# Kernel optimization log

Measured on AMD Instinct MI355X. Metric: run time of the kernel, lower is better.

The kernel has to match this reference:

```python
import jax, jax.numpy as jnp
import numpy as np

B, L, D, H, DH, S_POKES = 1, 4096, 1024, 16, 64, 3072


def setup_inputs() -> dict:
    key = jax.random.key(0)
    k0, k1, k2, k3 = jax.random.split(key, 4)
    x = jax.random.normal(k0, (B, L, D), jnp.float32)
    pos = jax.random.uniform(k1, (B, L, 2), jnp.float32)  # positions in [0,1]^2
    qkv_w = jax.random.normal(k2, (3 * D, D), jnp.float32) * 0.02
    out_w = jax.random.normal(k3, (D, D), jnp.float32) * 0.02
    scale = jnp.ones((H,), jnp.float32) * 10.0  # per-head cosine-sim scale (init 10)
    # AxialRoPE2D freq table: logspace(pi, 10*pi), view(2, d_head//4, n_heads).mT
    n = H * DH // 4
    f = np.exp(np.linspace(np.log(np.pi), np.log(10.0 * np.pi), n + 1)[:-1])
    freqs = jnp.asarray(np.stack([f, f]).reshape(2, DH // 4, H).transpose(0, 2, 1), jnp.float32)
    return {"x": x, "pos": pos, "qkv_w": qkv_w, "out_w": out_w,
            "scale": scale, "freqs": freqs, "n_pokes": S_POKES}


def _cos_scale(q, k, scale, eps=1e-8):
    # scale_for_cosine_sim: qk logits = scale * cosine_similarity
    sq = jnp.sum(q * q, axis=-1, keepdims=True)
    sk = jnp.sum(k * k, axis=-1, keepdims=True)
    ss = jnp.sqrt(jnp.abs(scale) + eps)
    return q * (ss * jax.lax.rsqrt(sq + eps)), k * (ss * jax.lax.rsqrt(sk + eps))


def _axial_theta(pos, freqs):
    # pos [B,L,2] in [0,1]; theta [B,H,L,DH//2]
    th_w = (pos[..., None, 0:1] * 2.0 - 1.0) * freqs[0]  # [B,L,H,DH//4]
    th_h = (pos[..., None, 1:2] * 2.0 - 1.0) * freqs[1]
    return jnp.concatenate([th_h, th_w], axis=-1).transpose(0, 2, 1, 3)


def _rope(x, theta):
    d = theta.shape[-1]  # DH//2 -> rotates the full head dim, x3 part empty
    x1, x2 = x[..., :d], x[..., d:2 * d]
    cos, sin = jnp.cos(theta), jnp.sin(theta)
    return jnp.concatenate([x1 * cos - x2 * sin, x2 * cos + x1 * sin], axis=-1)


def reference(x, pos, qkv_w, out_w, scale, freqs, n_pokes):
    b, l, dm = x.shape
    qkv = x @ qkv_w.T                          # [B,L,3D]
    q, k, v = jnp.split(qkv, 3, axis=-1)
    split_heads = lambda t: t.reshape(b, l, H, DH).transpose(0, 2, 1, 3)  # [B,H,L,DH]
    q, k, v = split_heads(q), split_heads(k), split_heads(v)
    q, k = _cos_scale(q, k, scale.reshape(1, H, 1, 1))
    theta = _axial_theta(pos, freqs)
    q, k = _rope(q, theta), _rope(k, theta)
    s = n_pokes
    qp, kp, vp = q[:, :, :s], k[:, :, :s], v[:, :, :s]
    qq, kq, vq = q[:, :, s:], k[:, :, s:], v[:, :, s:]
    # pokes: causal self-attention (scale=1.0, cosine-sim logits)
    sc_pp = jnp.einsum('bhqd,bhkd->bhqk', qp, kp)
    causal = jnp.tril(jnp.ones((s, s), bool))
    p_pp = jax.nn.softmax(jnp.where(causal, sc_pp, -jnp.inf), axis=-1)
    out_p = jnp.einsum('bhqk,bhkd->bhqd', p_pp, vp)
    # queries: attend to all pokes + themselves (diagonal), never each other
    sc_qp = jnp.einsum('bhqd,bhkd->bhqk', qq, kp)          # [B,H,Q,S]
    sc_self = jnp.sum(qq * kq, axis=-1, keepdims=True)     # [B,H,Q,1]
    p_q = jax.nn.softmax(jnp.concatenate([sc_qp, sc_self], axis=-1), axis=-1)
    out_q = jnp.einsum('bhqk,bhkd->bhqd', p_q[..., :s], vp) + p_q[..., s:] * vq
    out = jnp.concatenate([out_p, out_q], axis=2).transpose(0, 2, 1, 3).reshape(b, l, dm)
    return out @ out_w.T
```

## Files before the change

### kernel.cpp

```cpp
#include <hip/hip_runtime.h>
#include <math.h>

#define SEQL   4096
#define DMODEL 1024
#define NH     16
#define DHEAD  64
#define SPOKES 3072
#define NQUERY (SEQL - SPOKES)
#define QKVN   (3 * DMODEL)
#define LOG2E  1.4426950408889634f

typedef short bf16x8 __attribute__((ext_vector_type(8)));
typedef short bf16x4 __attribute__((ext_vector_type(4)));
typedef float f32x4  __attribute__((ext_vector_type(4)));

__device__ __forceinline__ short f2bf(float f) {
    unsigned u = __builtin_bit_cast(unsigned, f);
    u += 0x7fffu + ((u >> 16) & 1u);
    return (short)(u >> 16);
}
__device__ __forceinline__ float bf2f(short s) {
    unsigned u = ((unsigned)(unsigned short)s) << 16;
    return __builtin_bit_cast(float, u);
}
__device__ __forceinline__ unsigned cvt_pk_bf16(float lo, float hi) {
    unsigned u;
    asm("v_cvt_pk_bf16_f32 %0, %1, %2" : "=v"(u) : "v"(lo), "v"(hi));
    return u;
}
__device__ __forceinline__ float fast_exp2(float x) {
#if __has_builtin(__builtin_amdgcn_exp2f)
    return __builtin_amdgcn_exp2f(x);
#else
    float r; asm("v_exp_f32 %0, %1" : "=v"(r) : "v"(x)); return r;
#endif
}
__device__ __forceinline__ int swz(int row) { return ((row & 7) ^ (row >> 3)) << 4; }

__device__ __forceinline__ void gload_lds16(const void* g, void* l) {
    __builtin_amdgcn_global_load_lds(
        (const __attribute__((address_space(1))) unsigned int*)g,
        (__attribute__((address_space(3))) unsigned int*)l,
        16, 0, 0);
}

#define CVT_N0 (SEQL * DMODEL / 8)
#define CVT_N1 (QKVN * DMODEL / 8)
#define CVT_N2 (DMODEL * DMODEL / 8)
__global__ __launch_bounds__(256) void cvt_all(
    const float* __restrict__ x, const float* __restrict__ wq, const float* __restrict__ wo,
    short* __restrict__ xb, short* __restrict__ wqb, short* __restrict__ wob)
{
    int i = blockIdx.x * 256 + threadIdx.x;
    const float* src; short* dst;
    if (i < CVT_N0)               { src = x;  dst = xb; }
    else if (i < CVT_N0 + CVT_N1) { src = wq; dst = wqb; i -= CVT_N0; }
    else                          { src = wo; dst = wob; i -= CVT_N0 + CVT_N1; }
    float4 a = ((const float4*)src)[i * 2];
    float4 b = ((const float4*)src)[i * 2 + 1];
    bf16x8 v;
    v[0] = f2bf(a.x); v[1] = f2bf(a.y); v[2] = f2bf(a.z); v[3] = f2bf(a.w);
    v[4] = f2bf(b.x); v[5] = f2bf(b.y); v[6] = f2bf(b.z); v[7] = f2bf(b.w);
    ((bf16x8*)dst)[i] = v;
}

template<bool BF16OUT>
__global__ __launch_bounds__(256) void gemm_bf16(
    const short* __restrict__ A, const short* __restrict__ B, void* __restrict__ Cv,
    int K, int ldc)
{
    __shared__ short As[128 * 64];
    __shared__ short Bs[128 * 64];

    const int t = threadIdx.x;
    const int lane = t & 63, w = t >> 6;
    const int c = lane & 15, g = lane >> 4;
    const int wr = w >> 1, wc = w & 1;
    const int m0 = blockIdx.y * 128, n0 = blockIdx.x * 128;

    f32x4 acc[4][4] = {};

    for (int k0 = 0; k0 < K; k0 += 64) {
        __syncthreads();
        #pragma unroll
        for (int i = 0; i < 4; ++i) {
            const int chunk = (w * 4 + i) * 64 + lane;
            const int row = chunk >> 3, cc = chunk & 7;
            gload_lds16(A + (size_t)(m0 + row) * K + k0 + cc * 8,
                        As + (size_t)(w * 4 + i) * 512);
            gload_lds16(B + (size_t)(n0 + row) * K + k0 + cc * 8,
                        Bs + (size_t)(w * 4 + i) * 512);
        }
        __syncthreads();

        #pragma unroll
        for (int kk = 0; kk < 2; ++kk) {
            bf16x8 af[4], bf[4];
            #pragma unroll
            for (int i = 0; i < 4; ++i)
                af[i] = *(const bf16x8*)(As + (wr * 64 + i * 16 + c) * 64 + kk * 32 + g * 8);
            #pragma unroll
            for (int j = 0; j < 4; ++j)
                bf[j] = *(const bf16x8*)(Bs + (wc * 64 + j * 16 + c) * 64 + kk * 32 + g * 8);
            #pragma unroll
            for (int i = 0; i < 4; ++i)
                #pragma unroll
                for (int j = 0; j < 4; ++j)
                    acc[i][j] = __builtin_amdgcn_mfma_f32_16x16x32_bf16(af[i], bf[j], acc[i][j], 0, 0, 0);
        }
    }

    #pragma unroll
    for (int i = 0; i < 4; ++i)
        #pragma unroll
        for (int r = 0; r < 4; ++r) {
            const int row = m0 + wr * 64 + i * 16 + g * 4 + r;
            #pragma unroll
            for (int j = 0; j < 4; ++j) {
                const int col = n0 + wc * 64 + j * 16 + c;
                const float v = acc[i][j][r];
                if (BF16OUT) ((short*)Cv)[(size_t)row * ldc + col] = f2bf(v);
                else         ((float*)Cv)[(size_t)row * ldc + col] = v;
            }
        }
}

__global__ __launch_bounds__(256) void transform_qk(
    short* __restrict__ qkv, const float* __restrict__ pos,
    const float* __restrict__ scale, const float* __restrict__ freqs)
{
    const int w    = threadIdx.x >> 6;
    const int lane = threadIdx.x & 63;
    const int rid  = blockIdx.x * 4 + w;
    const int l    = rid >> 4;
    const int h    = rid & 15;

    short* qp = qkv + (size_t)l * QKVN + h * DHEAD;
    short* kp = qp + DMODEL;

    float q = bf2f(qp[lane]);
    float k = bf2f(kp[lane]);

    float sq = q * q, sk = k * k;
    #pragma unroll
    for (int o = 32; o > 0; o >>= 1) {
        sq += __shfl_xor(sq, o);
        sk += __shfl_xor(sk, o);
    }
    const float ss = sqrtf(fabsf(scale[h]) + 1e-8f);
    q *= ss * rsqrtf(sq + 1e-8f);
    k *= ss * rsqrtf(sk + 1e-8f);

    const int   j  = lane & 31;
    const float p  = pos[l * 2 + (j < 16 ? 1 : 0)];
    const float fj = (j < 16) ? freqs[256 + h * 16 + j] : freqs[h * 16 + (j - 16)];
    const float th = (p * 2.0f - 1.0f) * fj;
    const float cs = cosf(th), sn = sinf(th);

    const float qo = __shfl_xor(q, 32);
    const float ko = __shfl_xor(k, 32);
    const float qr = (lane < 32) ? q * cs - qo * sn : q * cs + qo * sn;
    const float kr = (lane < 32) ? k * cs - ko * sn : k * cs + ko * sn;

    qp[lane] = f2bf(qr * LOG2E);
    kp[lane] = f2bf(kr);
}

__global__ __launch_bounds__(256) void attn_fused(
    const short* __restrict__ qkv, const float* __restrict__ scale,
    short* __restrict__ attn,
    short* __restrict__ pacc_c, float* __restrict__ pml_c, float* __restrict__ pml0_c,
    short* __restrict__ pacc_q, float* __restrict__ pml_q, float* __restrict__ pml0_q)
{
    __shared__ short Kl[64 * 64];
    __shared__ short VTl[64 * 64];
    __shared__ short Pl[4][16 * 64];

    const int h = blockIdx.y;
    const int t = threadIdx.x, lane = t & 63, w = t >> 6;
    const int c = lane & 15, g = lane >> 4;
    const int qcol = h * DHEAD, kcol = DMODEL + h * DHEAD, vcol = 2 * DMODEL + h * DHEAD;

    const int xc = blockIdx.x;
    bool causal; int z, NS, q0, kt0, ktn, qt = 0, qb = 0;
    if (xc < 48) {
        causal = false; qb = xc / 3; z = xc - qb * 3; NS = 3;
        q0 = SPOKES + qb * 64; kt0 = z * 16; ktn = 16;
    } else {
        causal = true;
        if (xc < 96)       { const int i = xc - 48; qt = 47 - i / 3; z = i - (i / 3) * 3; NS = 3; }
        else if (xc < 128) { const int i = xc - 96; qt = 31 - (i >> 1); z = i & 1; NS = 2; }
        else               { qt = 143 - xc; z = 0; NS = 1; }
        q0 = qt * 64;
        const int full = qt + 1, b = full / NS, r = full - b * NS;
        kt0 = z * b + (z < r ? z : r);
        ktn = b + (z < r ? 1 : 0);
    }

    const int qg = q0 + w * 16 + c;

    const float Mlog = (fabsf(scale[h]) * 1.02f + 0.5f) * LOG2E;
    const f32x4 negM4 = {-Mlog, -Mlog, -Mlog, -Mlog};

    bf16x8 qf0, qf1;
    {
        const short* qrow = qkv + (size_t)qg * QKVN + qcol;
        qf0 = *(const bf16x8*)(qrow + g * 8);
        qf1 = *(const bf16x8*)(qrow + 32 + g * 8);
    }

    float l = 0.0f;
    f32x4 acc[4] = {};
    bf16x8 vregA, vregB;

    auto KDMA = [&](int kt) {
        const int k0 = kt * 64;
        #pragma unroll
        for (int i = 0; i < 2; ++i) {
            const int ch = i * 256 + t;
            const int kv = ch >> 3, s = ch & 7;
            const int o = s ^ ((kv & 7) ^ (kv >> 3));
            gload_lds16(qkv + (size_t)(k0 + kv) * QKVN + kcol + o * 8,
                        (char*)Kl + i * 4096 + w * 1024);
        }
    };
    auto VLOAD = [&](int kt) {
        const int k0 = kt * 64;
        const short* v0 = qkv + (size_t)(k0 + 2 * (t >> 3)) * QKVN + vcol + (t & 7) * 8;
        vregA = *(const bf16x8*)v0;
        vregB = *(const bf16x8*)(v0 + QKVN);
    };
    auto VWRITE = [&]() {
        const int p2 = t >> 3, oc = t & 7;
        #pragma unroll
        for (int j = 0; j < 8; ++j) {
            const int d = oc * 8 + j;
            const unsigned u = ((unsigned)(unsigned short)vregA[j]) |
                               (((unsigned)(unsigned short)vregB[j]) << 16);
            *(unsigned*)((char*)VTl + d * 128 + ((4 * p2) ^ swz(d))) = u;
        }
    };

    VLOAD(kt0);
    KDMA(kt0);
    VWRITE();
    __syncthreads();

    for (int it = 0; it < ktn; ++it) {
        const int kt = kt0 + it;
        const int k0 = kt * 64;

        f32x4 st[4];
        __builtin_amdgcn_s_setprio(1);
        #pragma unroll
        for (int mt = 0; mt < 4; ++mt) {
            const int kvr = mt * 16 + c;
            bf16x8 ka = *(const bf16x8*)((const char*)Kl + kvr * 128 + ((g * 16) ^ swz(kvr)));
            bf16x8 kb = *(const bf16x8*)((const char*)Kl + kvr * 128 + ((64 + g * 16) ^ swz(kvr)));
            f32x4 zz = __builtin_amdgcn_mfma_f32_16x16x32_bf16(ka, qf0, negM4, 0, 0, 0);
            st[mt] = __builtin_amdgcn_mfma_f32_16x16x32_bf16(kb, qf1, zz, 0, 0, 0);
        }
        __builtin_amdgcn_s_setprio(0);

        __syncthreads();
        if (it + 1 < ktn) { KDMA(kt + 1); VLOAD(kt + 1); }

        if (causal && (k0 + 63 > q0 + w * 16)) {
            #pragma unroll
            for (int mt = 0; mt < 4; ++mt)
                #pragma unroll
                for (int r = 0; r < 4; ++r)
                    if (k0 + mt * 16 + g * 4 + r > qg) st[mt][r] = -INFINITY;
        }
        {
            float rs = 0.0f;
            #pragma unroll
            for (int mt = 0; mt < 4; ++mt) {
                const float e0 = fast_exp2(st[mt][0]);
                const float e1 = fast_exp2(st[mt][1]);
                const float e2 = fast_exp2(st[mt][2]);
                const float e3 = fast_exp2(st[mt][3]);
                rs += (e0 + e1) + (e2 + e3);
                uint2 u;
                u.x = cvt_pk_bf16(e0, e1);
                u.y = cvt_pk_bf16(e2, e3);
                *(uint2*)((char*)Pl[w] + c * 128 + ((mt * 32 + g * 8) ^ swz(c))) = u;
            }
            rs += __shfl_xor(rs, 16);
            rs += __shfl_xor(rs, 32);
            l += rs;
        }

        __builtin_amdgcn_s_setprio(1);
        #pragma unroll
        for (int kc = 0; kc < 2; ++kc) {
            bf16x8 pb = *(const bf16x8*)((const char*)Pl[w] + c * 128 + ((kc * 64 + g * 16) ^ swz(c)));
            #pragma unroll
            for (int dt = 0; dt < 4; ++dt) {
                const int d = dt * 16 + c;
                bf16x8 vf = *(const bf16x8*)((const char*)VTl + d * 128 + ((kc * 64 + g * 16) ^ swz(d)));
                acc[dt] = __builtin_amdgcn_mfma_f32_16x16x32_bf16(vf, pb, acc[dt], 0, 0, 0);
            }
        }
        __builtin_amdgcn_s_setprio(0);

        __syncthreads();
        if (it + 1 < ktn) {
            VWRITE();
            __syncthreads();
        }
    }

    if (!causal && z == 0) {
        float ssv = 0.0f;
        {
            const short* krow = qkv + (size_t)qg * QKVN + kcol;
            bf16x8 k0s = *(const bf16x8*)(krow + g * 8);
            bf16x8 k1s = *(const bf16x8*)(krow + 32 + g * 8);
            #pragma unroll
            for (int j = 0; j < 8; ++j)
                ssv += bf2f(qf0[j]) * bf2f(k0s[j]) + bf2f(qf1[j]) * bf2f(k1s[j]);
            ssv += __shfl_xor(ssv, 16);
            ssv += __shfl_xor(ssv, 32);
        }
        const float ps = fast_exp2(ssv - Mlog);
        const short* vrow = qkv + (size_t)qg * QKVN + vcol;
        #pragma unroll
        for (int dt = 0; dt < 4; ++dt) {
            bf16x4 vs = *(const bf16x4*)(vrow + dt * 16 + g * 4);
            #pragma unroll
            for (int r = 0; r < 4; ++r)
                acc[dt][r] += ps * bf2f(vs[r]);
        }
        l += ps;
    }

    if (causal && NS == 1) {
        const float inv = 1.0f / l;
        short* orow = attn + (size_t)qg * DMODEL + qcol;
        #pragma unroll
        for (int dt = 0; dt < 4; ++dt)
            #pragma unroll
            for (int r = 0; r < 4; ++r)
                orow[dt * 16 + g * 4 + r] = f2bf(acc[dt][r] * inv);
    } else if (z == 0) {
        float* pml0 = causal ? pml0_c : pml0_q;
        const int stride = causal ? 2048 : 1024;
        const int base   = causal ? 1024 : SPOKES;
        short* orow = attn + (size_t)qg * DMODEL + qcol;
        #pragma unroll
        for (int dt = 0; dt < 4; ++dt)
            #pragma unroll
            for (int r = 0; r < 4; ++r)
                orow[dt * 16 + g * 4 + r] = f2bf(acc[dt][r]);
        if (g == 0) {
            float* p = pml0 + ((size_t)h * stride + (qg - base)) * 2;
            p[0] = Mlog;
            p[1] = l;
        }
    } else {
        const int slot = causal ? (qt < 32 ? qt - 16 : 16 + (qt - 32) * 2 + (z - 1))
                                : qb * 2 + (z - 1);
        short* pacc = causal ? pacc_c : pacc_q;
        float* pml  = causal ? pml_c  : pml_q;
        const int rl = w * 16 + c;
        short* prow = pacc + ((size_t)slot * 64 + rl) * DMODEL + qcol;
        #pragma unroll
        for (int dt = 0; dt < 4; ++dt)
            #pragma unroll
            for (int r = 0; r < 4; ++r)
                prow[dt * 16 + g * 4 + r] = f2bf(acc[dt][r]);
        if (g == 0) {
            float* p = pml + ((size_t)(slot * 16 + h) * 64 + rl) * 2;
            p[0] = Mlog;
            p[1] = l;
        }
    }
}

__global__ __launch_bounds__(256) void attn_combine_all(
    short* __restrict__ attn,
    const float* __restrict__ pml0_c, const short* __restrict__ pacc_c, const float* __restrict__ pml_c,
    const float* __restrict__ pml0_q, const short* __restrict__ pacc_q, const float* __restrict__ pml_q)
{
    const int gi = blockIdx.x * 256 + threadIdx.x;
    const int seg = gi >> 17;
    const int li  = gi & 131071;
    const int r = li >> 7;
    const int h = (li >> 3) & 15;
    const int o = li & 7;

    int rowbase, pml0_stride, pml0_off, slotBase, slotMul, nextra;
    const float* pml0; const short* pacc; const float* pml;
    if (seg == 0) {
        rowbase = 1024;   pml0_stride = 2048; pml0_off = 0;
        slotBase = 0;  slotMul = 1; nextra = 1;
        pml0 = pml0_c; pacc = pacc_c; pml = pml_c;
    } else if (seg == 1) {
        rowbase = 2048;   pml0_stride = 2048; pml0_off = 1024;
        slotBase = 16; slotMul = 2; nextra = 2;
        pml0 = pml0_c; pacc = pacc_c; pml = pml_c;
    } else {
        rowbase = SPOKES; pml0_stride = 1024; pml0_off = 0;
        slotBase = 0;  slotMul = 2; nextra = 2;
        pml0 = pml0_q; pacc = pacc_q; pml = pml_q;
    }

    const float* p0 = pml0 + ((size_t)h * pml0_stride + pml0_off + r) * 2;
    const float m0 = p0[0], l0 = p0[1];
    float M = m0;
    float me[2], le[2];
    for (int e = 0; e < nextra; ++e) {
        const int slot = slotBase + (r >> 6) * slotMul + e;
        const float* p = pml + ((size_t)(slot * 16 + h) * 64 + (r & 63)) * 2;
        me[e] = p[0]; le[e] = p[1];
        M = fmaxf(M, me[e]);
    }
    const float w0 = __expf(m0 - M);
    float L = w0 * l0;
    float we[2];
    for (int e = 0; e < nextra; ++e) { we[e] = __expf(me[e] - M); L += we[e] * le[e]; }

    short* arow = attn + (size_t)(rowbase + r) * DMODEL + h * 64 + o * 8;
    bf16x8 a0 = *(const bf16x8*)arow;
    float outv[8];
    #pragma unroll
    for (int j = 0; j < 8; ++j) outv[j] = w0 * bf2f(a0[j]);
    for (int e = 0; e < nextra; ++e) {
        const int slot = slotBase + (r >> 6) * slotMul + e;
        bf16x8 a = *(const bf16x8*)(pacc + ((size_t)slot * 64 + (r & 63)) * DMODEL + h * 64 + o * 8);
        #pragma unroll
        for (int j = 0; j < 8; ++j) outv[j] += we[e] * bf2f(a[j]);
    }
    const float inv = 1.0f / L;
    bf16x8 res;
    #pragma unroll
    for (int j = 0; j < 8; ++j) res[j] = f2bf(outv[j] * inv);
    *(bf16x8*)arow = res;
}

extern "C" void kernel_launch(void* const* d_in, const int* in_sizes, int n_in,
                              void* d_out, int out_size, void* d_ws, size_t ws_size,
                              hipStream_t stream)
{
    const float* x      = (const float*)d_in[0];
    const float* pos    = (const float*)d_in[1];
    const float* qkv_w  = (const float*)d_in[2];
    const float* out_w  = (const float*)d_in[3];
    const float* scale  = (const float*)d_in[4];
    const float* freqs  = (const float*)d_in[5];
    float*       out    = (float*)d_out;

    const size_t MB = 1024 * 1024;
    char* ws = (char*)d_ws;
    short* qkv_bf  = (short*)(ws);
    short* x_bf    = (short*)(ws + 24 * MB);
    short* wqkv_bf = (short*)(ws + 32 * MB);
    short* wout_bf = (short*)(ws + 38 * MB);
    short* pacc_c  = (short*)(ws + 40 * MB);
    float* pml_c   = (float*)(ws + 46 * MB);
    float* pml0_c  = (float*)(ws + 46 * MB + 393216);
    short* attn_bf = x_bf;
    short* pacc_q  = wqkv_bf;
    float* pml_q   = (float*)((char*)wqkv_bf + 4194304);
    float* pml0_q  = (float*)((char*)wqkv_bf + 4456448);

    const dim3 blk(256);

    cvt_all<<<dim3((CVT_N0 + CVT_N1 + CVT_N2) / 256), blk, 0, stream>>>(
        x, qkv_w, out_w, x_bf, wqkv_bf, wout_bf);

    gemm_bf16<true><<<dim3(QKVN / 128, SEQL / 128), blk, 0, stream>>>(
        x_bf, wqkv_bf, qkv_bf, DMODEL, QKVN);

    transform_qk<<<dim3(SEQL * NH / 4), blk, 0, stream>>>(qkv_bf, pos, scale, freqs);

    attn_fused<<<dim3(144, NH), blk, 0, stream>>>(
        qkv_bf, scale, attn_bf, pacc_c, pml_c, pml0_c, pacc_q, pml_q, pml0_q);

    attn_combine_all<<<dim3(1536), blk, 0, stream>>>(
        attn_bf, pml0_c, pacc_c, pml_c, pml0_q, pacc_q, pml_q);

    gemm_bf16<false><<<dim3(DMODEL / 128, SEQL / 128), blk, 0, stream>>>(
        attn_bf, wout_bf, out, DMODEL, DMODEL);
}
```

Measured before the change: 183.8 us.

## Double query tile per attention block to 128 rows, halving K/V reloads

Each attention block now processes 128 query rows (two 16-row fragments per wave) instead of 64, so each K/V tile staged in LDS feeds twice as many MFMAs. The grid shrinks from 144 to 72 blocks per head, and the causal split scheduling, partial-slot indexing and combine kernel are remapped to 128-row tiles. Causal fragments entirely above the diagonal skip their MFMAs. The cost is fewer blocks (1152 total), so occupancy and load balance drop, and register pressure rises from the doubled accumulators.

```diff
diff --git a/kernel.cpp b/kernel.cpp
--- a/kernel.cpp
+++ b/kernel.cpp
@@ -174,7 +174,7 @@
 {
     __shared__ short Kl[64 * 64];
     __shared__ short VTl[64 * 64];
-    __shared__ short Pl[4][16 * 64];
+    __shared__ short Pl[4][32 * 64];
 
     const int h = blockIdx.y;
     const int t = threadIdx.x, lane = t & 63, w = t >> 6;
@@ -183,34 +183,33 @@
 
     const int xc = blockIdx.x;
     bool causal; int z, NS, q0, kt0, ktn, qt = 0, qb = 0;
-    if (xc < 48) {
+    if (xc < 24) {
         causal = false; qb = xc / 3; z = xc - qb * 3; NS = 3;
-        q0 = SPOKES + qb * 64; kt0 = z * 16; ktn = 16;
+        q0 = SPOKES + qb * 128; kt0 = z * 16; ktn = 16;
     } else {
         causal = true;
-        if (xc < 96)       { const int i = xc - 48; qt = 47 - i / 3; z = i - (i / 3) * 3; NS = 3; }
-        else if (xc < 128) { const int i = xc - 96; qt = 31 - (i >> 1); z = i & 1; NS = 2; }
-        else               { qt = 143 - xc; z = 0; NS = 1; }
-        q0 = qt * 64;
-        const int full = qt + 1, b = full / NS, r = full - b * NS;
+        if (xc < 48)      { const int i = xc - 24; qt = 16 + i / 3; z = i - (i / 3) * 3; NS = 3; }
+        else if (xc < 64) { const int i = xc - 48; qt = 8 + (i >> 1); z = i & 1; NS = 2; }
+        else              { qt = 71 - xc; z = 0; NS = 1; }
+        q0 = qt * 128;
+        const int full = 2 * qt + 2, b = full / NS, r = full - b * NS;
         kt0 = z * b + (z < r ? z : r);
         ktn = b + (z < r ? 1 : 0);
     }
 
-    const int qg = q0 + w * 16 + c;
-
     const float Mlog = (fabsf(scale[h]) * 1.02f + 0.5f) * LOG2E;
     const f32x4 negM4 = {-Mlog, -Mlog, -Mlog, -Mlog};
 
-    bf16x8 qf0, qf1;
-    {
-        const short* qrow = qkv + (size_t)qg * QKVN + qcol;
-        qf0 = *(const bf16x8*)(qrow + g * 8);
-        qf1 = *(const bf16x8*)(qrow + 32 + g * 8);
-    }
-
-    float l = 0.0f;
-    f32x4 acc[4] = {};
+    bf16x8 qf[2][2];
+    #pragma unroll
+    for (int f = 0; f < 2; ++f) {
+        const short* qrow = qkv + (size_t)(q0 + w * 32 + f * 16 + c) * QKVN + qcol;
+        qf[f][0] = *(const bf16x8*)(qrow + g * 8);
+        qf[f][1] = *(const bf16x8*)(qrow + 32 + g * 8);
+    }
+
+    float l[2] = {0.0f, 0.0f};
+    f32x4 acc[2][4] = {};
     bf16x8 vregA, vregB;
 
     auto KDMA = [&](int kt) {
@@ -250,29 +249,43 @@
         const int kt = kt0 + it;
         const int k0 = kt * 64;
 
-        f32x4 st[4];
+        const bool live0 = !causal || (k0 <= q0 + w * 32 + 15);
+        const bool live1 = !causal || (k0 <= q0 + w * 32 + 31);
+
+        f32x4 st0[4], st1[4];
         __builtin_amdgcn_s_setprio(1);
         #pragma unroll
         for (int mt = 0; mt < 4; ++mt) {
             const int kvr = mt * 16 + c;
             bf16x8 ka = *(const bf16x8*)((const char*)Kl + kvr * 128 + ((g * 16) ^ swz(kvr)));
             bf16x8 kb = *(const bf16x8*)((const char*)Kl + kvr * 128 + ((64 + g * 16) ^ swz(kvr)));
-            f32x4 zz = __builtin_amdgcn_mfma_f32_16x16x32_bf16(ka, qf0, negM4, 0, 0, 0);
-            st[mt] = __builtin_amdgcn_mfma_f32_16x16x32_bf16(kb, qf1, zz, 0, 0, 0);
+            if (live0) {
+                f32x4 zz = __builtin_amdgcn_mfma_f32_16x16x32_bf16(ka, qf[0][0], negM4, 0, 0, 0);
+                st0[mt] = __builtin_amdgcn_mfma_f32_16x16x32_bf16(kb, qf[0][1], zz, 0, 0, 0);
+            }
+            if (live1) {
+                f32x4 zz = __builtin_amdgcn_mfma_f32_16x16x32_bf16(ka, qf[1][0], negM4, 0, 0, 0);
+                st1[mt] = __builtin_amdgcn_mfma_f32_16x16x32_bf16(kb, qf[1][1], zz, 0, 0, 0);
+            }
         }
         __builtin_amdgcn_s_setprio(0);
 
         __syncthreads();
         if (it + 1 < ktn) { KDMA(kt + 1); VLOAD(kt + 1); }
 
-        if (causal && (k0 + 63 > q0 + w * 16)) {
-            #pragma unroll
-            for (int mt = 0; mt < 4; ++mt)
-                #pragma unroll
-                for (int r = 0; r < 4; ++r)
-                    if (k0 + mt * 16 + g * 4 + r > qg) st[mt][r] = -INFINITY;
-        }
-        {
+        #pragma unroll
+        for (int f = 0; f < 2; ++f) {
+            if (f == 0 ? !live0 : !live1) continue;
+            f32x4* st = (f == 0) ? st0 : st1;
+            const int qrow = f * 16 + c;
+            const int qg = q0 + w * 32 + qrow;
+            if (causal && (k0 + 63 > q0 + w * 32 + f * 16)) {
+                #pragma unroll
+                for (int mt = 0; mt < 4; ++mt)
+                    #pragma unroll
+                    for (int r = 0; r < 4; ++r)
+                        if (k0 + mt * 16 + g * 4 + r > qg) st[mt][r] = -INFINITY;
+            }
             float rs = 0.0f;
             #pragma unroll
             for (int mt = 0; mt < 4; ++mt) {
@@ -284,22 +297,30 @@
                 uint2 u;
                 u.x = cvt_pk_bf16(e0, e1);
                 u.y = cvt_pk_bf16(e2, e3);
-                *(uint2*)((char*)Pl[w] + c * 128 + ((mt * 32 + g * 8) ^ swz(c))) = u;
+                *(uint2*)((char*)Pl[w] + qrow * 128 + ((mt * 32 + g * 8) ^ swz(qrow))) = u;
             }
             rs += __shfl_xor(rs, 16);
             rs += __shfl_xor(rs, 32);
-            l += rs;
+            l[f] += rs;
         }
 
         __builtin_amdgcn_s_setprio(1);
         #pragma unroll
         for (int kc = 0; kc < 2; ++kc) {
-            bf16x8 pb = *(const bf16x8*)((const char*)Pl[w] + c * 128 + ((kc * 64 + g * 16) ^ swz(c)));
+            bf16x8 vf[4];
             #pragma unroll
             for (int dt = 0; dt < 4; ++dt) {
                 const int d = dt * 16 + c;
-                bf16x8 vf = *(const bf16x8*)((const char*)VTl + d * 128 + ((kc * 64 + g * 16) ^ swz(d)));
-                acc[dt] = __builtin_amdgcn_mfma_f32_16x16x32_bf16(vf, pb, acc[dt], 0, 0, 0);
+                vf[dt] = *(const bf16x8*)((const char*)VTl + d * 128 + ((kc * 64 + g * 16) ^ swz(d)));
+            }
+            #pragma unroll
+            for (int f = 0; f < 2; ++f) {
+                if (f == 0 ? !live0 : !live1) continue;
+                const int qrow = f * 16 + c;
+                bf16x8 pb = *(const bf16x8*)((const char*)Pl[w] + qrow * 128 + ((kc * 64 + g * 16) ^ swz(qrow)));
+                #pragma unroll
+                for (int dt = 0; dt < 4; ++dt)
+                    acc[f][dt] = __builtin_amdgcn_mfma_f32_16x16x32_bf16(vf[dt], pb, acc[f][dt], 0, 0, 0);
             }
         }
         __builtin_amdgcn_s_setprio(0);
@@ -312,68 +333,82 @@
     }
 
     if (!causal && z == 0) {
-        float ssv = 0.0f;
-        {
-            const short* krow = qkv + (size_t)qg * QKVN + kcol;
-            bf16x8 k0s = *(const bf16x8*)(krow + g * 8);
-            bf16x8 k1s = *(const bf16x8*)(krow + 32 + g * 8);
-            #pragma unroll
-            for (int j = 0; j < 8; ++j)
-                ssv += bf2f(qf0[j]) * bf2f(k0s[j]) + bf2f(qf1[j]) * bf2f(k1s[j]);
-            ssv += __shfl_xor(ssv, 16);
-            ssv += __shfl_xor(ssv, 32);
-        }
-        const float ps = fast_exp2(ssv - Mlog);
-        const short* vrow = qkv + (size_t)qg * QKVN + vcol;
-        #pragma unroll
-        for (int dt = 0; dt < 4; ++dt) {
-            bf16x4 vs = *(const bf16x4*)(vrow + dt * 16 + g * 4);
-            #pragma unroll
-            for (int r = 0; r < 4; ++r)
-                acc[dt][r] += ps * bf2f(vs[r]);
-        }
-        l += ps;
+        #pragma unroll
+        for (int f = 0; f < 2; ++f) {
+            const int qg = q0 + w * 32 + f * 16 + c;
+            float ssv = 0.0f;
+            {
+                const short* krow = qkv + (size_t)qg * QKVN + kcol;
+                bf16x8 k0s = *(const bf16x8*)(krow + g * 8);
+                bf16x8 k1s = *(const bf16x8*)(krow + 32 + g * 8);
+                #pragma unroll
+                for (int j = 0; j < 8; ++j)
+                    ssv += bf2f(qf[f][0][j]) * bf2f(k0s[j]) + bf2f(qf[f][1][j]) * bf2f(k1s[j]);
+                ssv += __shfl_xor(ssv, 16);
+                ssv += __shfl_xor(ssv, 32);
+            }
+            const float ps = fast_exp2(ssv - Mlog);
+            const short* vrow = qkv + (size_t)qg * QKVN + vcol;
+            #pragma unroll
+            for (int dt = 0; dt < 4; ++dt) {
+                bf16x4 vs = *(const bf16x4*)(vrow + dt * 16 + g * 4);
+                #pragma unroll
+                for (int r = 0; r < 4; ++r)
+                    acc[f][dt][r] += ps * bf2f(vs[r]);
+            }
+            l[f] += ps;
+        }
     }
 
     if (causal && NS == 1) {
-        const float inv = 1.0f / l;
-        short* orow = attn + (size_t)qg * DMODEL + qcol;
-        #pragma unroll
-        for (int dt = 0; dt < 4; ++dt)
-            #pragma unroll
-            for (int r = 0; r < 4; ++r)
-                orow[dt * 16 + g * 4 + r] = f2bf(acc[dt][r] * inv);
+        #pragma unroll
+        for (int f = 0; f < 2; ++f) {
+            const float inv = 1.0f / l[f];
+            short* orow = attn + (size_t)(q0 + w * 32 + f * 16 + c) * DMODEL + qcol;
+            #pragma unroll
+            for (int dt = 0; dt < 4; ++dt)
+                #pragma unroll
+                for (int r = 0; r < 4; ++r)
+                    orow[dt * 16 + g * 4 + r] = f2bf(acc[f][dt][r] * inv);
+        }
     } else if (z == 0) {
         float* pml0 = causal ? pml0_c : pml0_q;
         const int stride = causal ? 2048 : 1024;
         const int base   = causal ? 1024 : SPOKES;
-        short* orow = attn + (size_t)qg * DMODEL + qcol;
-        #pragma unroll
-        for (int dt = 0; dt < 4; ++dt)
-            #pragma unroll
-            for (int r = 0; r < 4; ++r)
-                orow[dt * 16 + g * 4 + r] = f2bf(acc[dt][r]);
-        if (g == 0) {
-            float* p = pml0 + ((size_t)h * stride + (qg - base)) * 2;
-            p[0] = Mlog;
-            p[1] = l;
+        #pragma unroll
+        for (int f = 0; f < 2; ++f) {
+            const int row = q0 + w * 32 + f * 16 + c;
+            short* orow = attn + (size_t)row * DMODEL + qcol;
+            #pragma unroll
+            for (int dt = 0; dt < 4; ++dt)
+                #pragma unroll
+                for (int r = 0; r < 4; ++r)
+                    orow[dt * 16 + g * 4 + r] = f2bf(acc[f][dt][r]);
+            if (g == 0) {
+                float* p = pml0 + ((size_t)h * stride + (row - base)) * 2;
+                p[0] = Mlog;
+                p[1] = l[f];
+            }
         }
     } else {
-        const int slot = causal ? (qt < 32 ? qt - 16 : 16 + (qt - 32) * 2 + (z - 1))
+        const int slot = causal ? (qt < 16 ? qt - 8 : 8 + (qt - 16) * 2 + (z - 1))
                                 : qb * 2 + (z - 1);
         short* pacc = causal ? pacc_c : pacc_q;
         float* pml  = causal ? pml_c  : pml_q;
-        const int rl = w * 16 + c;
-        short* prow = pacc + ((size_t)slot * 64 + rl) * DMODEL + qcol;
-        #pragma unroll
-        for (int dt = 0; dt < 4; ++dt)
-            #pragma unroll
-            for (int r = 0; r < 4; ++r)
-                prow[dt * 16 + g * 4 + r] = f2bf(acc[dt][r]);
-        if (g == 0) {
-            float* p = pml + ((size_t)(slot * 16 + h) * 64 + rl) * 2;
-            p[0] = Mlog;
-            p[1] = l;
+        #pragma unroll
+        for (int f = 0; f < 2; ++f) {
+            const int rl = w * 32 + f * 16 + c;
+            short* prow = pacc + ((size_t)slot * 128 + rl) * DMODEL + qcol;
+            #pragma unroll
+            for (int dt = 0; dt < 4; ++dt)
+                #pragma unroll
+                for (int r = 0; r < 4; ++r)
+                    prow[dt * 16 + g * 4 + r] = f2bf(acc[f][dt][r]);
+            if (g == 0) {
+                float* p = pml + ((size_t)(slot * 16 + h) * 128 + rl) * 2;
+                p[0] = Mlog;
+                p[1] = l[f];
+            }
         }
     }
 }
@@ -398,7 +433,7 @@
         pml0 = pml0_c; pacc = pacc_c; pml = pml_c;
     } else if (seg == 1) {
         rowbase = 2048;   pml0_stride = 2048; pml0_off = 1024;
-        slotBase = 16; slotMul = 2; nextra = 2;
+        slotBase = 8;  slotMul = 2; nextra = 2;
         pml0 = pml0_c; pacc = pacc_c; pml = pml_c;
     } else {
         rowbase = SPOKES; pml0_stride = 1024; pml0_off = 0;
@@ -411,8 +446,8 @@
     float M = m0;
     float me[2], le[2];
     for (int e = 0; e < nextra; ++e) {
-        const int slot = slotBase + (r >> 6) * slotMul + e;
-        const float* p = pml + ((size_t)(slot * 16 + h) * 64 + (r & 63)) * 2;
+        const int slot = slotBase + (r >> 7) * slotMul + e;
+        const float* p = pml + ((size_t)(slot * 16 + h) * 128 + (r & 127)) * 2;
         me[e] = p[0]; le[e] = p[1];
         M = fmaxf(M, me[e]);
     }
@@ -427,8 +462,8 @@
     #pragma unroll
     for (int j = 0; j < 8; ++j) outv[j] = w0 * bf2f(a0[j]);
     for (int e = 0; e < nextra; ++e) {
-        const int slot = slotBase + (r >> 6) * slotMul + e;
-        bf16x8 a = *(const bf16x8*)(pacc + ((size_t)slot * 64 + (r & 63)) * DMODEL + h * 64 + o * 8);
+        const int slot = slotBase + (r >> 7) * slotMul + e;
+        bf16x8 a = *(const bf16x8*)(pacc + ((size_t)slot * 128 + (r & 127)) * DMODEL + h * 64 + o * 8);
         #pragma unroll
         for (int j = 0; j < 8; ++j) outv[j] += we[e] * bf2f(a[j]);
     }
@@ -475,7 +510,7 @@
 
     transform_qk<<<dim3(SEQL * NH / 4), blk, 0, stream>>>(qkv_bf, pos, scale, freqs);
 
-    attn_fused<<<dim3(144, NH), blk, 0, stream>>>(
+    attn_fused<<<dim3(72, NH), blk, 0, stream>>>(
         qkv_bf, scale, attn_bf, pacc_c, pml_c, pml0_c, pacc_q, pml_q, pml0_q);
 
     attn_combine_all<<<dim3(1536), blk, 0, stream>>>(
```

Result: slower. 194.3 us (+5.7%).
